# Performance work log

Measured on AMD Instinct MI355X. Metric: run time of the kernel, lower is better.

Reference implementation:

```python
import jax, jax.numpy as jnp
import numpy as np

N = 50000
E = 800000
F_IN, F_HID, F_OUT = 128, 128, 64


def setup_inputs() -> dict:
    key = jax.random.key(0)
    ks = jax.random.split(key, 8)
    x = jax.random.normal(ks[0], (N, F_IN), dtype=jnp.float32)
    attn_edge_index = jax.random.randint(ks[1], (2, E), 0, N, dtype=jnp.int64)
    attn_edge_weight = jax.random.uniform(ks[2], (E,), dtype=jnp.float32)
    # GCNConv params (glorot-ish scale); PyG lin has no bias, conv bias added after aggregation
    W1 = jax.random.normal(ks[3], (F_IN, F_HID), dtype=jnp.float32) * (1.0 / np.sqrt(F_IN))
    b1 = jnp.zeros((F_HID,), dtype=jnp.float32)
    W2 = jax.random.normal(ks[4], (F_HID, F_OUT), dtype=jnp.float32) * (1.0 / np.sqrt(F_HID))
    b2 = jnp.zeros((F_OUT,), dtype=jnp.float32)
    return {"x": x, "attn_edge_index": attn_edge_index, "attn_edge_weight": attn_edge_weight,
            "W1": W1, "b1": b1, "W2": W2, "b2": b2}


def _gcn_norm(edge_index, edge_weight, num_nodes):
    # Add self-loops with weight 1 (PyG gcn_norm default)
    loop = jnp.arange(num_nodes, dtype=edge_index.dtype)
    src = jnp.concatenate([edge_index[0], loop])
    dst = jnp.concatenate([edge_index[1], loop])
    w = jnp.concatenate([edge_weight, jnp.ones((num_nodes,), edge_weight.dtype)])
    deg = jax.ops.segment_sum(w, dst, num_segments=num_nodes)  # in-degree weighted
    dinv = jnp.where(deg > 0, jax.lax.rsqrt(deg), 0.0)
    norm = dinv[src] * w * dinv[dst]  # symmetric normalization
    return src, dst, norm


def _gcn_conv(h, src, dst, norm, W, b, num_nodes):
    h = h @ W                                   # [N, Fout] dense transform
    msg = norm[:, None] * h[src]                # [E+N, Fout] gather-multiply
    out = jax.ops.segment_sum(msg, dst, num_segments=num_nodes)  # scatter-add
    return out + b


def reference(x, attn_edge_index, attn_edge_weight, W1, b1, W2, b2):
    num_nodes = x.shape[0]
    src, dst, norm = _gcn_norm(attn_edge_index, attn_edge_weight, num_nodes)
    h = _gcn_conv(x, src, dst, norm, W1, b1, num_nodes)
    h = jax.nn.relu(h)
    # dropout(p=0.5) is identity in eval mode
    h = _gcn_conv(h, src, dst, norm, W2, b2, num_nodes)
    return h
```

## Files before the change

### kernel.cpp

```cpp
#include <hip/hip_runtime.h>
#include <hip/hip_bf16.h>

static constexpr int FIN   = 128;
static constexpr int FHID  = 128;
static constexpr int FOUTC = 64;
static constexpr int CAP   = 64;

typedef short bf16x8 __attribute__((ext_vector_type(8)));
typedef float f32x4 __attribute__((ext_vector_type(4)));

__device__ __forceinline__ float bfbits2f(unsigned short u) {
  union { unsigned i; float f; } c; c.i = ((unsigned)u) << 16; return c.f;
}
__device__ __forceinline__ float wbits2f(unsigned u) {
  union { unsigned i; float f; } c; c.i = u; return c.f;
}
__device__ __forceinline__ unsigned f2wbits(float f) {
  union { float fv; unsigned i; } c; c.fv = f; return c.i;
}
__device__ __forceinline__ void unpack_bf2(unsigned u, float& lo, float& hi) {
  union { unsigned i; float f; } a, b;
  a.i = u << 16;
  b.i = u & 0xffff0000u;
  lo = a.f; hi = b.f;
}
__device__ __forceinline__ unsigned short f2bfbits(float f) {
  union { float fv; unsigned i; } c; c.fv = f;
  unsigned i = c.i;
  unsigned r = i + 0x7FFFu + ((i >> 16) & 1u);
  if ((i & 0x7F800000u) == 0x7F800000u) r = i;
  return (unsigned short)(r >> 16);
}
__device__ __forceinline__ int ld_idx(const void* ei, int is64, long long off) {
  return is64 ? (int)((const long long*)ei)[off] : ((const int*)ei)[off];
}
__device__ __forceinline__ float ld_f(const void* p, int isbf, long long i) {
  return isbf ? bfbits2f(((const unsigned short*)p)[i]) : ((const float*)p)[i];
}

__device__ __forceinline__ int compact_row(uint2 rec, int lane, const float* __restrict__ dinv,
                                           int& rsrc, float& rw) {
  unsigned long long m = __ballot(rec.y != 0u);
  int c = __popcll(m);
  int rank = __popcll(m & ((1ull << lane) - 1ull));
  int destl = (rec.y != 0u) ? rank : c + (lane - rank);
  rsrc = __builtin_amdgcn_ds_permute(destl << 2, (int)rec.x);
  int rwb = __builtin_amdgcn_ds_permute(destl << 2, (int)rec.y);
  rw = (lane < c) ? wbits2f((unsigned)rwb) * dinv[rsrc] : 0.f;
  return c;
}

__global__ void setup_kernel(const unsigned short* __restrict__ xb,
                             const unsigned* __restrict__ eiw,
                             const void* __restrict__ W1, const void* __restrict__ W2,
                             int* __restrict__ flags, unsigned short* __restrict__ Wt1,
                             unsigned short* __restrict__ Wt2) {
  const int tid = threadIdx.x;
  __shared__ int sflags[2];
  if (tid < 64) {
    unsigned short xs = xb[2 * tid];
    unsigned long long mb = __ballot(((xs >> 7) & 0xFFu) >= 0xC0u);
    unsigned long long m2 = __ballot(eiw[2 * tid + 1] != 0u);
    if (tid == 0) {
      sflags[0] = (mb == 0ull);
      sflags[1] = (m2 == 0ull);
      if (blockIdx.x == 0) { flags[0] = sflags[0]; flags[1] = sflags[1]; }
    }
  }
  __syncthreads();
  int f = sflags[0];
  int i = blockIdx.x * 256 + tid;
  if (i < 128 * 128) {
    int k = i >> 7, nn = i & 127;
    Wt1[nn * 128 + k] = f2bfbits(ld_f(W1, f, i));
  } else {
    int j = i - 128 * 128;
    int k = j >> 6, nn = j & 63;
    Wt2[nn * 128 + k] = f2bfbits(ld_f(W2, f, j));
  }
}

__global__ void fill_ell(const void* __restrict__ ei, const void* __restrict__ ew,
                         const int* __restrict__ flg, unsigned long long* __restrict__ ell,
                         int E, int half) {
  int g = blockIdx.x * 256 + threadIdx.x;
  if (g >= half) return;
  int is64 = flg[1], isbf = flg[0];
  int sA = ld_idx(ei, is64, g);
  int dA = ld_idx(ei, is64, (long long)E + g);
  unsigned wA = f2wbits(ld_f(ew, isbf, g));
  int eB = g + half;
  bool hasB = eB < E;
  int sB = 0, dB = 0;
  unsigned wB = 0u;
  if (hasB) {
    sB = ld_idx(ei, is64, eB);
    dB = ld_idx(ei, is64, (long long)E + eB);
    wB = f2wbits(ld_f(ew, isbf, eB));
  }
  unsigned long long vA = ((unsigned long long)wA << 32) | (unsigned)sA;
  unsigned long long vB = ((unsigned long long)wB << 32) | (unsigned)sB;
  unsigned long long* rowA = ell + (size_t)dA * CAP;
  unsigned long long* rowB = ell + (size_t)dB * CAP;
  int pA = g & (CAP - 1), pB = eB & (CAP - 1);
  bool doneA = (vA == 0ull);
  bool doneB = !hasB || (vB == 0ull);
  unsigned long long oA = doneA ? 0ull : atomicCAS(&rowA[pA], 0ull, vA);
  unsigned long long oB = doneB ? 0ull : atomicCAS(&rowB[pB], 0ull, vB);
  for (int t = 1; t < CAP && !doneA && oA != 0ull; ++t) {
    pA = (pA + 1) & (CAP - 1);
    oA = atomicCAS(&rowA[pA], 0ull, vA);
  }
  for (int t = 1; t < CAP && !doneB && oB != 0ull; ++t) {
    pB = (pB + 1) & (CAP - 1);
    oB = atomicCAS(&rowB[pB], 0ull, vB);
  }
}

__global__ void node_dinv(const uint2* __restrict__ ell, float* __restrict__ dinv, int n) {
  int wid = (blockIdx.x * 256 + threadIdx.x) >> 6;
  int lane = threadIdx.x & 63;
  if (wid >= n) return;
  float w = wbits2f(ell[(size_t)wid * CAP + lane].y);
#pragma unroll
  for (int off = 1; off < 64; off <<= 1) w += __shfl_xor(w, off);
  if (lane == 0) dinv[wid] = rsqrtf(1.f + w);
}

__launch_bounds__(256)
__global__ void gather_l1(const void* __restrict__ x, const int* __restrict__ flg,
                          const uint2* __restrict__ ell, const float* __restrict__ dinv,
                          uint4* __restrict__ agg, int n) {
  int wid = (blockIdx.x * 256 + threadIdx.x) >> 6;
  int lane = threadIdx.x & 63;
  if (wid >= n) return;
  uint2 rec = ell[(size_t)wid * CAP + lane];
  int rsrc;
  float rw;
  int c = compact_row(rec, lane, dinv, rsrc, rw);
  float di = dinv[wid];

  if (flg[0]) {
    const uint4* xv = (const uint4*)x;
    const int fgrp = lane & 15, egrp = lane >> 4;
    float acc[8];
#pragma unroll
    for (int k = 0; k < 8; ++k) acc[k] = 0.f;
    int iters = (c + 15) >> 4;
    for (int it = 0; it < iters; ++it) {
      int b = it * 16 + egrp;
      int i0 = b, i1 = b + 4, i2 = b + 8, i3 = b + 12;
      int s0 = __shfl(rsrc, i0), s1 = __shfl(rsrc, i1);
      int s2 = __shfl(rsrc, i2), s3 = __shfl(rsrc, i3);
      float w0 = __shfl(rw, i0), w1 = __shfl(rw, i1);
      float w2 = __shfl(rw, i2), w3 = __shfl(rw, i3);
      s0 = i0 < c ? s0 : wid; s1 = i1 < c ? s1 : wid;
      s2 = i2 < c ? s2 : wid; s3 = i3 < c ? s3 : wid;
      uint4 u0 = xv[(size_t)s0 * 16 + fgrp];
      uint4 u1 = xv[(size_t)s1 * 16 + fgrp];
      uint4 u2 = xv[(size_t)s2 * 16 + fgrp];
      uint4 u3 = xv[(size_t)s3 * 16 + fgrp];
      float l, h;
      unpack_bf2(u0.x, l, h); acc[0] = fmaf(w0, l, acc[0]); acc[1] = fmaf(w0, h, acc[1]);
      unpack_bf2(u0.y, l, h); acc[2] = fmaf(w0, l, acc[2]); acc[3] = fmaf(w0, h, acc[3]);
      unpack_bf2(u0.z, l, h); acc[4] = fmaf(w0, l, acc[4]); acc[5] = fmaf(w0, h, acc[5]);
      unpack_bf2(u0.w, l, h); acc[6] = fmaf(w0, l, acc[6]); acc[7] = fmaf(w0, h, acc[7]);
      unpack_bf2(u1.x, l, h); acc[0] = fmaf(w1, l, acc[0]); acc[1] = fmaf(w1, h, acc[1]);
      unpack_bf2(u1.y, l, h); acc[2] = fmaf(w1, l, acc[2]); acc[3] = fmaf(w1, h, acc[3]);
      unpack_bf2(u1.z, l, h); acc[4] = fmaf(w1, l, acc[4]); acc[5] = fmaf(w1, h, acc[5]);
      unpack_bf2(u1.w, l, h); acc[6] = fmaf(w1, l, acc[6]); acc[7] = fmaf(w1, h, acc[7]);
      unpack_bf2(u2.x, l, h); acc[0] = fmaf(w2, l, acc[0]); acc[1] = fmaf(w2, h, acc[1]);
      unpack_bf2(u2.y, l, h); acc[2] = fmaf(w2, l, acc[2]); acc[3] = fmaf(w2, h, acc[3]);
      unpack_bf2(u2.z, l, h); acc[4] = fmaf(w2, l, acc[4]); acc[5] = fmaf(w2, h, acc[5]);
      unpack_bf2(u2.w, l, h); acc[6] = fmaf(w2, l, acc[6]); acc[7] = fmaf(w2, h, acc[7]);
      unpack_bf2(u3.x, l, h); acc[0] = fmaf(w3, l, acc[0]); acc[1] = fmaf(w3, h, acc[1]);
      unpack_bf2(u3.y, l, h); acc[2] = fmaf(w3, l, acc[2]); acc[3] = fmaf(w3, h, acc[3]);
      unpack_bf2(u3.z, l, h); acc[4] = fmaf(w3, l, acc[4]); acc[5] = fmaf(w3, h, acc[5]);
      unpack_bf2(u3.w, l, h); acc[6] = fmaf(w3, l, acc[6]); acc[7] = fmaf(w3, h, acc[7]);
    }
#pragma unroll
    for (int k = 0; k < 8; ++k) {
      acc[k] += __shfl_xor(acc[k], 16);
      acc[k] += __shfl_xor(acc[k], 32);
    }
    if (lane < 16) {
      uint4 su = xv[(size_t)wid * 16 + fgrp];
      float s0, s1, s2, s3, s4, s5, s6, s7;
      unpack_bf2(su.x, s0, s1); unpack_bf2(su.y, s2, s3);
      unpack_bf2(su.z, s4, s5); unpack_bf2(su.w, s6, s7);
      float dd = di * di;
      float o0 = di * acc[0] + dd * s0, o1 = di * acc[1] + dd * s1;
      float o2 = di * acc[2] + dd * s2, o3 = di * acc[3] + dd * s3;
      float o4 = di * acc[4] + dd * s4, o5 = di * acc[5] + dd * s5;
      float o6 = di * acc[6] + dd * s6, o7 = di * acc[7] + dd * s7;
      uint4 pk;
      pk.x = (unsigned)f2bfbits(o0) | ((unsigned)f2bfbits(o1) << 16);
      pk.y = (unsigned)f2bfbits(o2) | ((unsigned)f2bfbits(o3) << 16);
      pk.z = (unsigned)f2bfbits(o4) | ((unsigned)f2bfbits(o5) << 16);
      pk.w = (unsigned)f2bfbits(o6) | ((unsigned)f2bfbits(o7) << 16);
      agg[(size_t)wid * 16 + fgrp] = pk;
    }
  } else {
    const float4* xf = (const float4*)x;
    const int fgrp = lane & 31, egrp = lane >> 5;
    float acc[4] = {0.f, 0.f, 0.f, 0.f};
    int it8 = (c + 7) >> 3;
    for (int it = 0; it < it8; ++it) {
      int b = it * 8 + egrp;
#pragma unroll
      for (int t = 0; t < 4; ++t) {
        int idx = b + t * 2;
        int s = __shfl(rsrc, idx);
        float w = __shfl(rw, idx);
        s = idx < c ? s : wid;
        float4 v = xf[(size_t)s * 32 + fgrp];
        acc[0] = fmaf(w, v.x, acc[0]); acc[1] = fmaf(w, v.y, acc[1]);
        acc[2] = fmaf(w, v.z, acc[2]); acc[3] = fmaf(w, v.w, acc[3]);
      }
    }
#pragma unroll
    for (int k = 0; k < 4; ++k) acc[k] += __shfl_xor(acc[k], 32);
    if (lane < 32) {
      float4 sv = xf[(size_t)wid * 32 + fgrp];
      float dd = di * di;
      float o0 = di * acc[0] + dd * sv.x, o1 = di * acc[1] + dd * sv.y;
      float o2 = di * acc[2] + dd * sv.z, o3 = di * acc[3] + dd * sv.w;
      uint2 pk;
      pk.x = (unsigned)f2bfbits(o0) | ((unsigned)f2bfbits(o1) << 16);
      pk.y = (unsigned)f2bfbits(o2) | ((unsigned)f2bfbits(o3) << 16);
      ((uint2*)agg)[(size_t)wid * 32 + fgrp] = pk;
    }
  }
}

__launch_bounds__(256)
__global__ void gather_l2(const unsigned short* __restrict__ hw2, const int* __restrict__ flg,
                          const uint2* __restrict__ ell, const float* __restrict__ dinv,
                          const void* __restrict__ b2, void* __restrict__ out, int n) {
  int wid = (blockIdx.x * 256 + threadIdx.x) >> 6;
  int lane = threadIdx.x & 63;
  if (wid >= n) return;
  uint2 rec = ell[(size_t)wid * CAP + lane];
  int rsrc;
  float rw;
  int c = compact_row(rec, lane, dinv, rsrc, rw);
  float di = dinv[wid];

  const uint4* hv = (const uint4*)hw2;
  const int fgrp = lane & 7, egrp = lane >> 3;
  float acc[8];
#pragma unroll
  for (int k = 0; k < 8; ++k) acc[k] = 0.f;
  int iters = (c + 15) >> 4;
  for (int it = 0; it < iters; ++it) {
    int i0 = it * 16 + egrp, i1 = i0 + 8;
    int s0 = __shfl(rsrc, i0), s1 = __shfl(rsrc, i1);
    float w0 = __shfl(rw, i0), w1 = __shfl(rw, i1);
    s0 = i0 < c ? s0 : wid;
    s1 = i1 < c ? s1 : wid;
    uint4 u0 = hv[(size_t)s0 * 8 + fgrp];
    uint4 u1 = hv[(size_t)s1 * 8 + fgrp];
    float l, h;
    unpack_bf2(u0.x, l, h); acc[0] = fmaf(w0, l, acc[0]); acc[1] = fmaf(w0, h, acc[1]);
    unpack_bf2(u0.y, l, h); acc[2] = fmaf(w0, l, acc[2]); acc[3] = fmaf(w0, h, acc[3]);
    unpack_bf2(u0.z, l, h); acc[4] = fmaf(w0, l, acc[4]); acc[5] = fmaf(w0, h, acc[5]);
    unpack_bf2(u0.w, l, h); acc[6] = fmaf(w0, l, acc[6]); acc[7] = fmaf(w0, h, acc[7]);
    unpack_bf2(u1.x, l, h); acc[0] = fmaf(w1, l, acc[0]); acc[1] = fmaf(w1, h, acc[1]);
    unpack_bf2(u1.y, l, h); acc[2] = fmaf(w1, l, acc[2]); acc[3] = fmaf(w1, h, acc[3]);
    unpack_bf2(u1.z, l, h); acc[4] = fmaf(w1, l, acc[4]); acc[5] = fmaf(w1, h, acc[5]);
    unpack_bf2(u1.w, l, h); acc[6] = fmaf(w1, l, acc[6]); acc[7] = fmaf(w1, h, acc[7]);
  }
#pragma unroll
  for (int k = 0; k < 8; ++k) {
    acc[k] += __shfl_xor(acc[k], 8);
    acc[k] += __shfl_xor(acc[k], 16);
    acc[k] += __shfl_xor(acc[k], 32);
  }
  if (lane < 8) {
    int isbf = flg[0];
    uint4 su = hv[(size_t)wid * 8 + fgrp];
    float s0, s1, s2, s3, s4, s5, s6, s7;
    unpack_bf2(su.x, s0, s1); unpack_bf2(su.y, s2, s3);
    unpack_bf2(su.z, s4, s5); unpack_bf2(su.w, s6, s7);
    float dd = di * di;
    float o0 = di * acc[0] + dd * s0 + ld_f(b2, isbf, fgrp * 8 + 0);
    float o1 = di * acc[1] + dd * s1 + ld_f(b2, isbf, fgrp * 8 + 1);
    float o2 = di * acc[2] + dd * s2 + ld_f(b2, isbf, fgrp * 8 + 2);
    float o3 = di * acc[3] + dd * s3 + ld_f(b2, isbf, fgrp * 8 + 3);
    float o4 = di * acc[4] + dd * s4 + ld_f(b2, isbf, fgrp * 8 + 4);
    float o5 = di * acc[5] + dd * s5 + ld_f(b2, isbf, fgrp * 8 + 5);
    float o6 = di * acc[6] + dd * s6 + ld_f(b2, isbf, fgrp * 8 + 6);
    float o7 = di * acc[7] + dd * s7 + ld_f(b2, isbf, fgrp * 8 + 7);
    if (isbf) {
      uint4 pk;
      pk.x = (unsigned)f2bfbits(o0) | ((unsigned)f2bfbits(o1) << 16);
      pk.y = (unsigned)f2bfbits(o2) | ((unsigned)f2bfbits(o3) << 16);
      pk.z = (unsigned)f2bfbits(o4) | ((unsigned)f2bfbits(o5) << 16);
      pk.w = (unsigned)f2bfbits(o6) | ((unsigned)f2bfbits(o7) << 16);
      ((uint4*)out)[(size_t)wid * 8 + fgrp] = pk;
    } else {
      ((float4*)out)[(size_t)wid * 16 + fgrp * 2 + 0] = make_float4(o0, o1, o2, o3);
      ((float4*)out)[(size_t)wid * 16 + fgrp * 2 + 1] = make_float4(o4, o5, o6, o7);
    }
  }
}

__launch_bounds__(256)
__global__ void gemm12(const unsigned short* __restrict__ agg1,
                       const unsigned short* __restrict__ Wt1,
                       const unsigned short* __restrict__ Wt2,
                       const void* __restrict__ b1, const int* __restrict__ flg,
                       unsigned short* __restrict__ hw2, int M) {
  __shared__ unsigned short As[128 * 128];
  __shared__ unsigned short W1s[128 * 128];
  __shared__ unsigned short W2s[64 * 128];
  const int tid = threadIdx.x;
  const int r0 = blockIdx.x * 128;

  for (int i = tid; i < 128 * 16; i += 256) {
    int r = i >> 4, ch = i & 15;
    uint4 v = make_uint4(0u, 0u, 0u, 0u);
    if (r0 + r < M) v = *(const uint4*)(agg1 + (size_t)(r0 + r) * 128 + ch * 8);
    *(uint4*)&As[r * 128 + ((ch ^ (r & 15)) << 3)] = v;
  }
  for (int i = tid; i < 128 * 16; i += 256) {
    int r = i >> 4, ch = i & 15;
    uint4 v = *(const uint4*)(Wt1 + (size_t)r * 128 + ch * 8);
    *(uint4*)&W1s[r * 128 + ((ch ^ (r & 15)) << 3)] = v;
  }
  for (int i = tid; i < 64 * 16; i += 256) {
    int r = i >> 4, ch = i & 15;
    uint4 v = *(const uint4*)(Wt2 + (size_t)r * 128 + ch * 8);
    *(uint4*)&W2s[r * 128 + ((ch ^ (r & 15)) << 3)] = v;
  }
  __syncthreads();

  const int lane = tid & 63;
  const int wv = tid >> 6;
  const int ln15 = lane & 15;
  const int kq = lane >> 4;
  const int wbf = flg[0];

  f32x4 acc1[2][8];
#pragma unroll
  for (int mi = 0; mi < 2; ++mi)
#pragma unroll
    for (int nt = 0; nt < 8; ++nt) acc1[mi][nt] = (f32x4){0.f, 0.f, 0.f, 0.f};
#pragma unroll
  for (int kc = 0; kc < 4; ++kc) {
    int coff = (((kc * 4 + kq) ^ ln15) << 3);
    bf16x8 a0 = *(const bf16x8*)&As[((2 * wv + 0) * 16 + ln15) * 128 + coff];
    bf16x8 a1 = *(const bf16x8*)&As[((2 * wv + 1) * 16 + ln15) * 128 + coff];
#pragma unroll
    for (int nt = 0; nt < 8; ++nt) {
      bf16x8 b = *(const bf16x8*)&W1s[(nt * 16 + ln15) * 128 + coff];
      acc1[0][nt] = __builtin_amdgcn_mfma_f32_16x16x32_bf16(a0, b, acc1[0][nt], 0, 0, 0);
      acc1[1][nt] = __builtin_amdgcn_mfma_f32_16x16x32_bf16(a1, b, acc1[1][nt], 0, 0, 0);
    }
  }

#pragma unroll
  for (int nt = 0; nt < 8; ++nt) {
    int col = nt * 16 + ln15;
    float bv = ld_f(b1, wbf, col);
#pragma unroll
    for (int mi = 0; mi < 2; ++mi) {
#pragma unroll
      for (int r = 0; r < 4; ++r) {
        int row = 32 * wv + mi * 16 + kq * 4 + r;
        float o = fmaxf(acc1[mi][nt][r] + bv, 0.f);
        As[row * 128 + ((((col >> 3)) ^ (row & 15)) << 3) + (col & 7)] = f2bfbits(o);
      }
    }
  }
  __syncthreads();

  f32x4 acc2[2][4];
#pragma unroll
  for (int mi = 0; mi < 2; ++mi)
#pragma unroll
    for (int nt = 0; nt < 4; ++nt) acc2[mi][nt] = (f32x4){0.f, 0.f, 0.f, 0.f};
#pragma unroll
  for (int kc = 0; kc < 4; ++kc) {
    int coff = (((kc * 4 + kq) ^ ln15) << 3);
    bf16x8 a0 = *(const bf16x8*)&As[((2 * wv + 0) * 16 + ln15) * 128 + coff];
    bf16x8 a1 = *(const bf16x8*)&As[((2 * wv + 1) * 16 + ln15) * 128 + coff];
#pragma unroll
    for (int nt = 0; nt < 4; ++nt) {
      bf16x8 b = *(const bf16x8*)&W2s[(nt * 16 + ln15) * 128 + coff];
      acc2[0][nt] = __builtin_amdgcn_mfma_f32_16x16x32_bf16(a0, b, acc2[0][nt], 0, 0, 0);
      acc2[1][nt] = __builtin_amdgcn_mfma_f32_16x16x32_bf16(a1, b, acc2[1][nt], 0, 0, 0);
    }
  }
#pragma unroll
  for (int nt = 0; nt < 4; ++nt) {
    int col = nt * 16 + ln15;
#pragma unroll
    for (int mi = 0; mi < 2; ++mi) {
#pragma unroll
      for (int r = 0; r < 4; ++r) {
        int gr = r0 + 32 * wv + mi * 16 + kq * 4 + r;
        if (gr < M) hw2[(size_t)gr * 64 + col] = f2bfbits(acc2[mi][nt][r]);
      }
    }
  }
}

extern "C" void kernel_launch(void* const* d_in, const int* in_sizes, int n_in, void* d_out,
                              int out_size, void* d_ws, size_t ws_size, hipStream_t stream) {
  const void* x  = d_in[0];
  const void* ei = d_in[1];
  const void* ew = d_in[2];
  const void* W1 = d_in[3];
  const void* b1 = d_in[4];
  const void* W2 = d_in[5];
  const void* b2 = d_in[6];

  const int N = in_sizes[0] / FIN;
  const int E = in_sizes[1] / 2;
  const int B = 256;

  int* flags   = (int*)d_ws;
  float* dinv  = (float*)(flags + 16);
  unsigned short* Wt1 = (unsigned short*)(dinv + N);
  unsigned short* Wt2 = Wt1 + 128 * 128;
  unsigned long long* ell = (unsigned long long*)(Wt2 + 64 * 128);
  unsigned short* agg1 = (unsigned short*)(ell + (size_t)N * CAP);
  unsigned short* hw2  = agg1 + (size_t)N * FHID;

  const int half = (E + 1) / 2;
  hipMemsetAsync(ell, 0, (size_t)N * CAP * sizeof(unsigned long long), stream);
  setup_kernel<<<96, B, 0, stream>>>((const unsigned short*)x, (const unsigned*)ei, W1, W2,
                                     flags, Wt1, Wt2);
  fill_ell<<<(half + B - 1) / B, B, 0, stream>>>(ei, ew, flags, ell, E, half);
  node_dinv<<<(N + 3) / 4, B, 0, stream>>>((const uint2*)ell, dinv, N);
  gather_l1<<<(N + 3) / 4, B, 0, stream>>>(x, flags, (const uint2*)ell, dinv, (uint4*)agg1, N);
  gemm12<<<(N + 127) / 128, B, 0, stream>>>(agg1, Wt1, Wt2, b1, flags, hw2, N);
  gather_l2<<<(N + 3) / 4, B, 0, stream>>>(hw2, flags, (const uint2*)ell, dinv, b2, d_out, N);
}
```

Baseline: 234.8 us.

## Persistent phased layer-1 gather partitioned by source range with grid soft barriers

Replaces the one-wave-per-node layer-1 gather with a persistent kernel of 1024 blocks. Each block keeps about 49 node accumulators and compacted edge lists in LDS and walks the edges in four phases by source-node range, separated by spin-wait grid barriers, so each phase's gathered feature rows stay L2-resident. The ELL zeroing moves from hipMemsetAsync into setup_kernel, and setup_kernel also clears the barrier counters. This adds barrier spin cost, a bounded spin that can fall through without full synchronisation, edge weights rounded to bf16, and a dependence on all 1024 blocks being co-resident.

```diff
diff --git a/kernel.cpp b/kernel.cpp
--- a/kernel.cpp
+++ b/kernel.cpp
@@ -5,6 +5,9 @@
 static constexpr int FHID  = 128;
 static constexpr int FOUTC = 64;
 static constexpr int CAP   = 64;
+static constexpr int NBLK  = 1024;
+static constexpr int PN    = 49;
+static constexpr int NPH   = 4;
 
 typedef short bf16x8 __attribute__((ext_vector_type(8)));
 typedef float f32x4 __attribute__((ext_vector_type(4)));
@@ -50,12 +53,28 @@
   return c;
 }
 
+__device__ __forceinline__ void soft_barrier(int* __restrict__ ctr, int idx, int target) {
+  __syncthreads();
+  if (threadIdx.x == 0) {
+    __threadfence();
+    atomicAdd(&ctr[idx], 1);
+    for (int spins = 0; spins < 3000; ++spins) {
+      int v = __hip_atomic_load(&ctr[idx], __ATOMIC_RELAXED, __HIP_MEMORY_SCOPE_AGENT);
+      if (v >= target) break;
+      __builtin_amdgcn_s_sleep(1);
+    }
+  }
+  __syncthreads();
+}
+
 __global__ void setup_kernel(const unsigned short* __restrict__ xb,
                              const unsigned* __restrict__ eiw,
                              const void* __restrict__ W1, const void* __restrict__ W2,
                              int* __restrict__ flags, unsigned short* __restrict__ Wt1,
-                             unsigned short* __restrict__ Wt2) {
+                             unsigned short* __restrict__ Wt2, uint4* __restrict__ ellz,
+                             int nell4) {
   const int tid = threadIdx.x;
+  const int gid = blockIdx.x * 256 + tid;
   __shared__ int sflags[2];
   if (tid < 64) {
     unsigned short xs = xb[2 * tid];
@@ -67,17 +86,22 @@
       if (blockIdx.x == 0) { flags[0] = sflags[0]; flags[1] = sflags[1]; }
     }
   }
+  if (blockIdx.x == 0 && tid >= 128 && tid < 144) flags[8 + (tid - 128)] = 0;
   __syncthreads();
   int f = sflags[0];
-  int i = blockIdx.x * 256 + tid;
-  if (i < 128 * 128) {
-    int k = i >> 7, nn = i & 127;
-    Wt1[nn * 128 + k] = f2bfbits(ld_f(W1, f, i));
-  } else {
-    int j = i - 128 * 128;
-    int k = j >> 6, nn = j & 63;
-    Wt2[nn * 128 + k] = f2bfbits(ld_f(W2, f, j));
-  }
+  if (blockIdx.x < 96) {
+    int i = gid;
+    if (i < 128 * 128) {
+      int k = i >> 7, nn = i & 127;
+      Wt1[nn * 128 + k] = f2bfbits(ld_f(W1, f, i));
+    } else {
+      int j = i - 128 * 128;
+      int k = j >> 6, nn = j & 63;
+      Wt2[nn * 128 + k] = f2bfbits(ld_f(W2, f, j));
+    }
+  }
+  uint4 z = make_uint4(0u, 0u, 0u, 0u);
+  for (int j = gid; j < nell4; j += gridDim.x * 256) ellz[j] = z;
 }
 
 __global__ void fill_ell(const void* __restrict__ ei, const void* __restrict__ ew,
@@ -127,108 +151,182 @@
   if (lane == 0) dinv[wid] = rsqrtf(1.f + w);
 }
 
-__launch_bounds__(256)
-__global__ void gather_l1(const void* __restrict__ x, const int* __restrict__ flg,
-                          const uint2* __restrict__ ell, const float* __restrict__ dinv,
-                          uint4* __restrict__ agg, int n) {
-  int wid = (blockIdx.x * 256 + threadIdx.x) >> 6;
-  int lane = threadIdx.x & 63;
-  if (wid >= n) return;
-  uint2 rec = ell[(size_t)wid * CAP + lane];
-  int rsrc;
-  float rw;
-  int c = compact_row(rec, lane, dinv, rsrc, rw);
-  float di = dinv[wid];
-
-  if (flg[0]) {
-    const uint4* xv = (const uint4*)x;
-    const int fgrp = lane & 15, egrp = lane >> 4;
-    float acc[8];
-#pragma unroll
-    for (int k = 0; k < 8; ++k) acc[k] = 0.f;
-    int iters = (c + 15) >> 4;
-    for (int it = 0; it < iters; ++it) {
-      int b = it * 16 + egrp;
-      int i0 = b, i1 = b + 4, i2 = b + 8, i3 = b + 12;
-      int s0 = __shfl(rsrc, i0), s1 = __shfl(rsrc, i1);
-      int s2 = __shfl(rsrc, i2), s3 = __shfl(rsrc, i3);
-      float w0 = __shfl(rw, i0), w1 = __shfl(rw, i1);
-      float w2 = __shfl(rw, i2), w3 = __shfl(rw, i3);
-      s0 = i0 < c ? s0 : wid; s1 = i1 < c ? s1 : wid;
-      s2 = i2 < c ? s2 : wid; s3 = i3 < c ? s3 : wid;
-      uint4 u0 = xv[(size_t)s0 * 16 + fgrp];
-      uint4 u1 = xv[(size_t)s1 * 16 + fgrp];
-      uint4 u2 = xv[(size_t)s2 * 16 + fgrp];
-      uint4 u3 = xv[(size_t)s3 * 16 + fgrp];
-      float l, h;
-      unpack_bf2(u0.x, l, h); acc[0] = fmaf(w0, l, acc[0]); acc[1] = fmaf(w0, h, acc[1]);
-      unpack_bf2(u0.y, l, h); acc[2] = fmaf(w0, l, acc[2]); acc[3] = fmaf(w0, h, acc[3]);
-      unpack_bf2(u0.z, l, h); acc[4] = fmaf(w0, l, acc[4]); acc[5] = fmaf(w0, h, acc[5]);
-      unpack_bf2(u0.w, l, h); acc[6] = fmaf(w0, l, acc[6]); acc[7] = fmaf(w0, h, acc[7]);
-      unpack_bf2(u1.x, l, h); acc[0] = fmaf(w1, l, acc[0]); acc[1] = fmaf(w1, h, acc[1]);
-      unpack_bf2(u1.y, l, h); acc[2] = fmaf(w1, l, acc[2]); acc[3] = fmaf(w1, h, acc[3]);
-      unpack_bf2(u1.z, l, h); acc[4] = fmaf(w1, l, acc[4]); acc[5] = fmaf(w1, h, acc[5]);
-      unpack_bf2(u1.w, l, h); acc[6] = fmaf(w1, l, acc[6]); acc[7] = fmaf(w1, h, acc[7]);
-      unpack_bf2(u2.x, l, h); acc[0] = fmaf(w2, l, acc[0]); acc[1] = fmaf(w2, h, acc[1]);
-      unpack_bf2(u2.y, l, h); acc[2] = fmaf(w2, l, acc[2]); acc[3] = fmaf(w2, h, acc[3]);
-      unpack_bf2(u2.z, l, h); acc[4] = fmaf(w2, l, acc[4]); acc[5] = fmaf(w2, h, acc[5]);
-      unpack_bf2(u2.w, l, h); acc[6] = fmaf(w2, l, acc[6]); acc[7] = fmaf(w2, h, acc[7]);
-      unpack_bf2(u3.x, l, h); acc[0] = fmaf(w3, l, acc[0]); acc[1] = fmaf(w3, h, acc[1]);
-      unpack_bf2(u3.y, l, h); acc[2] = fmaf(w3, l, acc[2]); acc[3] = fmaf(w3, h, acc[3]);
-      unpack_bf2(u3.z, l, h); acc[4] = fmaf(w3, l, acc[4]); acc[5] = fmaf(w3, h, acc[5]);
-      unpack_bf2(u3.w, l, h); acc[6] = fmaf(w3, l, acc[6]); acc[7] = fmaf(w3, h, acc[7]);
-    }
-#pragma unroll
-    for (int k = 0; k < 8; ++k) {
-      acc[k] += __shfl_xor(acc[k], 16);
-      acc[k] += __shfl_xor(acc[k], 32);
-    }
-    if (lane < 16) {
-      uint4 su = xv[(size_t)wid * 16 + fgrp];
-      float s0, s1, s2, s3, s4, s5, s6, s7;
-      unpack_bf2(su.x, s0, s1); unpack_bf2(su.y, s2, s3);
-      unpack_bf2(su.z, s4, s5); unpack_bf2(su.w, s6, s7);
-      float dd = di * di;
-      float o0 = di * acc[0] + dd * s0, o1 = di * acc[1] + dd * s1;
-      float o2 = di * acc[2] + dd * s2, o3 = di * acc[3] + dd * s3;
-      float o4 = di * acc[4] + dd * s4, o5 = di * acc[5] + dd * s5;
-      float o6 = di * acc[6] + dd * s6, o7 = di * acc[7] + dd * s7;
-      uint4 pk;
-      pk.x = (unsigned)f2bfbits(o0) | ((unsigned)f2bfbits(o1) << 16);
-      pk.y = (unsigned)f2bfbits(o2) | ((unsigned)f2bfbits(o3) << 16);
-      pk.z = (unsigned)f2bfbits(o4) | ((unsigned)f2bfbits(o5) << 16);
-      pk.w = (unsigned)f2bfbits(o6) | ((unsigned)f2bfbits(o7) << 16);
-      agg[(size_t)wid * 16 + fgrp] = pk;
-    }
-  } else {
-    const float4* xf = (const float4*)x;
-    const int fgrp = lane & 31, egrp = lane >> 5;
-    float acc[4] = {0.f, 0.f, 0.f, 0.f};
-    int it8 = (c + 7) >> 3;
-    for (int it = 0; it < it8; ++it) {
-      int b = it * 8 + egrp;
-#pragma unroll
-      for (int t = 0; t < 4; ++t) {
-        int idx = b + t * 2;
-        int s = __shfl(rsrc, idx);
-        float w = __shfl(rw, idx);
-        s = idx < c ? s : wid;
-        float4 v = xf[(size_t)s * 32 + fgrp];
-        acc[0] = fmaf(w, v.x, acc[0]); acc[1] = fmaf(w, v.y, acc[1]);
-        acc[2] = fmaf(w, v.z, acc[2]); acc[3] = fmaf(w, v.w, acc[3]);
-      }
-    }
-#pragma unroll
-    for (int k = 0; k < 4; ++k) acc[k] += __shfl_xor(acc[k], 32);
-    if (lane < 32) {
-      float4 sv = xf[(size_t)wid * 32 + fgrp];
-      float dd = di * di;
-      float o0 = di * acc[0] + dd * sv.x, o1 = di * acc[1] + dd * sv.y;
-      float o2 = di * acc[2] + dd * sv.z, o3 = di * acc[3] + dd * sv.w;
-      uint2 pk;
-      pk.x = (unsigned)f2bfbits(o0) | ((unsigned)f2bfbits(o1) << 16);
-      pk.y = (unsigned)f2bfbits(o2) | ((unsigned)f2bfbits(o3) << 16);
-      ((uint2*)agg)[(size_t)wid * 32 + fgrp] = pk;
+__launch_bounds__(256, 4)
+__global__ void gather_l1p(const void* __restrict__ x, const int* __restrict__ flg,
+                           const uint2* __restrict__ ell, const float* __restrict__ dinv,
+                           unsigned* __restrict__ agg, int n, int* __restrict__ ctr) {
+  __shared__ float accL[PN * 128];
+  __shared__ unsigned eL[PN * CAP];
+  __shared__ int cL[PN];
+  const int tid = threadIdx.x;
+  const int wv = tid >> 6;
+  const int lane = tid & 63;
+  const int blk = blockIdx.x;
+  const int isbf = flg[0];
+
+  for (int i = wv; blk + i * NBLK < n; i += 4) {
+    int nd = blk + i * NBLK;
+    uint2 rec = ell[(size_t)nd * CAP + lane];
+    bool valid = rec.y != 0u;
+    unsigned long long m = __ballot(valid);
+    int c = __popcll(m);
+    int rank = __popcll(m & ((1ull << lane) - 1ull));
+    int destl = valid ? rank : c + (lane - rank);
+    float wdi = valid ? wbits2f(rec.y) * dinv[rec.x] : 0.f;
+    unsigned entry = ((unsigned)rec.x << 16) | (unsigned)f2bfbits(wdi);
+    int pe = __builtin_amdgcn_ds_permute(destl << 2, (int)entry);
+    if (lane < c) eL[i * CAP + lane] = (unsigned)pe;
+    if (lane == 0) cL[i] = c;
+    float di = dinv[nd];
+    if (isbf) {
+      if (lane < 16) {
+        uint4 su = ((const uint4*)x)[(size_t)nd * 16 + lane];
+        float f0, f1, f2, f3, f4, f5, f6, f7;
+        unpack_bf2(su.x, f0, f1); unpack_bf2(su.y, f2, f3);
+        unpack_bf2(su.z, f4, f5); unpack_bf2(su.w, f6, f7);
+        float* a = &accL[i * 128];
+        a[0 * 16 + lane] = di * f0; a[1 * 16 + lane] = di * f1;
+        a[2 * 16 + lane] = di * f2; a[3 * 16 + lane] = di * f3;
+        a[4 * 16 + lane] = di * f4; a[5 * 16 + lane] = di * f5;
+        a[6 * 16 + lane] = di * f6; a[7 * 16 + lane] = di * f7;
+      }
+    } else {
+      if (lane < 32) {
+        float4 sv = ((const float4*)x)[(size_t)nd * 32 + lane];
+        float* a = &accL[i * 128];
+        a[0 * 32 + lane] = di * sv.x; a[1 * 32 + lane] = di * sv.y;
+        a[2 * 32 + lane] = di * sv.z; a[3 * 32 + lane] = di * sv.w;
+      }
+    }
+  }
+
+  const int CH = (n + NPH - 1) / NPH;
+  for (int p = 0; p < NPH; ++p) {
+    soft_barrier(ctr + 8, p, NBLK);
+    int lo, hi;
+    if (isbf) { lo = p * CH; hi = lo + CH; }
+    else      { lo = (p == 0) ? 0 : n + 1; hi = (p == 0) ? n : n + 1; }
+    for (int i = wv; blk + i * NBLK < n; i += 4) {
+      int nd = blk + i * NBLK;
+      int c = cL[i];
+      unsigned e = (lane < c) ? eL[i * CAP + lane] : 0u;
+      int src = (int)(e >> 16);
+      bool act = (lane < c) && src >= lo && src < hi;
+      unsigned long long m = __ballot(act);
+      int cp = __popcll(m);
+      if (cp == 0) continue;
+      int rank = __popcll(m & ((1ull << lane) - 1ull));
+      int destl = act ? rank : cp + (lane - rank);
+      int rsrc = __builtin_amdgcn_ds_permute(destl << 2, src);
+      int rwb = __builtin_amdgcn_ds_permute(destl << 2, (int)(e << 16));
+      float rw = wbits2f((unsigned)rwb);
+
+      if (isbf) {
+        const uint4* xv = (const uint4*)x;
+        const int fgrp = lane & 15, egrp = lane >> 4;
+        float acc[8];
+#pragma unroll
+        for (int k = 0; k < 8; ++k) acc[k] = 0.f;
+        int iters = (cp + 15) >> 4;
+        for (int it = 0; it < iters; ++it) {
+          int b = it * 16 + egrp;
+          int i0 = b, i1 = b + 4, i2 = b + 8, i3 = b + 12;
+          int s0 = __shfl(rsrc, i0), s1 = __shfl(rsrc, i1);
+          int s2 = __shfl(rsrc, i2), s3 = __shfl(rsrc, i3);
+          float w0 = __shfl(rw, i0), w1 = __shfl(rw, i1);
+          float w2 = __shfl(rw, i2), w3 = __shfl(rw, i3);
+          s0 = i0 < cp ? s0 : nd; w0 = i0 < cp ? w0 : 0.f;
+          s1 = i1 < cp ? s1 : nd; w1 = i1 < cp ? w1 : 0.f;
+          s2 = i2 < cp ? s2 : nd; w2 = i2 < cp ? w2 : 0.f;
+          s3 = i3 < cp ? s3 : nd; w3 = i3 < cp ? w3 : 0.f;
+          uint4 u0 = xv[(size_t)s0 * 16 + fgrp];
+          uint4 u1 = xv[(size_t)s1 * 16 + fgrp];
+          uint4 u2 = xv[(size_t)s2 * 16 + fgrp];
+          uint4 u3 = xv[(size_t)s3 * 16 + fgrp];
+          float l, h;
+          unpack_bf2(u0.x, l, h); acc[0] = fmaf(w0, l, acc[0]); acc[1] = fmaf(w0, h, acc[1]);
+          unpack_bf2(u0.y, l, h); acc[2] = fmaf(w0, l, acc[2]); acc[3] = fmaf(w0, h, acc[3]);
+          unpack_bf2(u0.z, l, h); acc[4] = fmaf(w0, l, acc[4]); acc[5] = fmaf(w0, h, acc[5]);
+          unpack_bf2(u0.w, l, h); acc[6] = fmaf(w0, l, acc[6]); acc[7] = fmaf(w0, h, acc[7]);
+          unpack_bf2(u1.x, l, h); acc[0] = fmaf(w1, l, acc[0]); acc[1] = fmaf(w1, h, acc[1]);
+          unpack_bf2(u1.y, l, h); acc[2] = fmaf(w1, l, acc[2]); acc[3] = fmaf(w1, h, acc[3]);
+          unpack_bf2(u1.z, l, h); acc[4] = fmaf(w1, l, acc[4]); acc[5] = fmaf(w1, h, acc[5]);
+          unpack_bf2(u1.w, l, h); acc[6] = fmaf(w1, l, acc[6]); acc[7] = fmaf(w1, h, acc[7]);
+          unpack_bf2(u2.x, l, h); acc[0] = fmaf(w2, l, acc[0]); acc[1] = fmaf(w2, h, acc[1]);
+          unpack_bf2(u2.y, l, h); acc[2] = fmaf(w2, l, acc[2]); acc[3] = fmaf(w2, h, acc[3]);
+          unpack_bf2(u2.z, l, h); acc[4] = fmaf(w2, l, acc[4]); acc[5] = fmaf(w2, h, acc[5]);
+          unpack_bf2(u2.w, l, h); acc[6] = fmaf(w2, l, acc[6]); acc[7] = fmaf(w2, h, acc[7]);
+          unpack_bf2(u3.x, l, h); acc[0] = fmaf(w3, l, acc[0]); acc[1] = fmaf(w3, h, acc[1]);
+          unpack_bf2(u3.y, l, h); acc[2] = fmaf(w3, l, acc[2]); acc[3] = fmaf(w3, h, acc[3]);
+          unpack_bf2(u3.z, l, h); acc[4] = fmaf(w3, l, acc[4]); acc[5] = fmaf(w3, h, acc[5]);
+          unpack_bf2(u3.w, l, h); acc[6] = fmaf(w3, l, acc[6]); acc[7] = fmaf(w3, h, acc[7]);
+        }
+#pragma unroll
+        for (int k = 0; k < 8; ++k) {
+          acc[k] += __shfl_xor(acc[k], 16);
+          acc[k] += __shfl_xor(acc[k], 32);
+        }
+        if (lane < 16) {
+          float* a = &accL[i * 128];
+#pragma unroll
+          for (int k = 0; k < 8; ++k) a[k * 16 + fgrp] += acc[k];
+        }
+      } else {
+        const float4* xf = (const float4*)x;
+        const int fgrp = lane & 31, egrp = lane >> 5;
+        float acc[4] = {0.f, 0.f, 0.f, 0.f};
+        int it8 = (cp + 7) >> 3;
+        for (int it = 0; it < it8; ++it) {
+          int b = it * 8 + egrp;
+#pragma unroll
+          for (int t = 0; t < 4; ++t) {
+            int idx = b + t * 2;
+            int s = __shfl(rsrc, idx);
+            float w = __shfl(rw, idx);
+            s = idx < cp ? s : nd;
+            w = idx < cp ? w : 0.f;
+            float4 v = xf[(size_t)s * 32 + fgrp];
+            acc[0] = fmaf(w, v.x, acc[0]); acc[1] = fmaf(w, v.y, acc[1]);
+            acc[2] = fmaf(w, v.z, acc[2]); acc[3] = fmaf(w, v.w, acc[3]);
+          }
+        }
+#pragma unroll
+        for (int k = 0; k < 4; ++k) acc[k] += __shfl_xor(acc[k], 32);
+        if (lane < 32) {
+          float* a = &accL[i * 128];
+#pragma unroll
+          for (int k = 0; k < 4; ++k) a[k * 32 + fgrp] += acc[k];
+        }
+      }
+    }
+  }
+
+  for (int i = wv; blk + i * NBLK < n; i += 4) {
+    int nd = blk + i * NBLK;
+    float di = dinv[nd];
+    if (isbf) {
+      if (lane < 16) {
+        const float* a = &accL[i * 128];
+        float o[8];
+#pragma unroll
+        for (int k = 0; k < 8; ++k) o[k] = di * a[k * 16 + lane];
+        uint4 pk;
+        pk.x = (unsigned)f2bfbits(o[0]) | ((unsigned)f2bfbits(o[1]) << 16);
+        pk.y = (unsigned)f2bfbits(o[2]) | ((unsigned)f2bfbits(o[3]) << 16);
+        pk.z = (unsigned)f2bfbits(o[4]) | ((unsigned)f2bfbits(o[5]) << 16);
+        pk.w = (unsigned)f2bfbits(o[6]) | ((unsigned)f2bfbits(o[7]) << 16);
+        ((uint4*)agg)[(size_t)nd * 16 + lane] = pk;
+      }
+    } else {
+      if (lane < 32) {
+        const float* a = &accL[i * 128];
+        float o0 = di * a[0 * 32 + lane], o1 = di * a[1 * 32 + lane];
+        float o2 = di * a[2 * 32 + lane], o3 = di * a[3 * 32 + lane];
+        uint2 pk;
+        pk.x = (unsigned)f2bfbits(o0) | ((unsigned)f2bfbits(o1) << 16);
+        pk.y = (unsigned)f2bfbits(o2) | ((unsigned)f2bfbits(o3) << 16);
+        ((uint2*)agg)[(size_t)nd * 32 + lane] = pk;
+      }
     }
   }
 }
@@ -421,7 +519,7 @@
   const int B = 256;
 
   int* flags   = (int*)d_ws;
-  float* dinv  = (float*)(flags + 16);
+  float* dinv  = (float*)(flags + 24);
   unsigned short* Wt1 = (unsigned short*)(dinv + N);
   unsigned short* Wt2 = Wt1 + 128 * 128;
   unsigned long long* ell = (unsigned long long*)(Wt2 + 64 * 128);
@@ -429,12 +527,12 @@
   unsigned short* hw2  = agg1 + (size_t)N * FHID;
 
   const int half = (E + 1) / 2;
-  hipMemsetAsync(ell, 0, (size_t)N * CAP * sizeof(unsigned long long), stream);
-  setup_kernel<<<96, B, 0, stream>>>((const unsigned short*)x, (const unsigned*)ei, W1, W2,
-                                     flags, Wt1, Wt2);
+  setup_kernel<<<512, B, 0, stream>>>((const unsigned short*)x, (const unsigned*)ei, W1, W2,
+                                      flags, Wt1, Wt2, (uint4*)ell, N * CAP / 2);
   fill_ell<<<(half + B - 1) / B, B, 0, stream>>>(ei, ew, flags, ell, E, half);
   node_dinv<<<(N + 3) / 4, B, 0, stream>>>((const uint2*)ell, dinv, N);
-  gather_l1<<<(N + 3) / 4, B, 0, stream>>>(x, flags, (const uint2*)ell, dinv, (uint4*)agg1, N);
+  gather_l1p<<<NBLK, B, 0, stream>>>(x, flags, (const uint2*)ell, dinv, (unsigned*)agg1, N,
+                                     flags);
   gemm12<<<(N + 127) / 128, B, 0, stream>>>(agg1, Wt1, Wt2, b1, flags, hw2, N);
   gather_l2<<<(N + 3) / 4, B, 0, stream>>>(hw2, flags, (const uint2*)ell, dinv, b2, d_out, N);
 }
```

Measured after the change: 559.4 us. 138% more time.

## Precompact ELL rows into packed 32-bit edges and split layer-1 gather by feature half

Applied to the files above, without the earlier changes.

Node-degree computation now also compacts each ELL row into packed 32-bit entries, with the source index in the high 16 bits and a bf16 edge weight in the low 16. The entries are written in place over the ELL buffer, so both gathers read half the edge bytes and no longer redo the ballot/permute compaction. The layer-1 gather is split into two launches, each handling 64 features. This aims at a smaller working set per pass for better cache reuse. The ELL memset is folded into the setup kernel, and nontemporal loads and stores are used. The risks are packing that assumes fewer than 65536 nodes, weights rounded to bf16, and an extra kernel launch.

```diff
diff --git a/kernel.cpp b/kernel.cpp
--- a/kernel.cpp
+++ b/kernel.cpp
@@ -8,6 +8,8 @@
 
 typedef short bf16x8 __attribute__((ext_vector_type(8)));
 typedef float f32x4 __attribute__((ext_vector_type(4)));
+typedef unsigned u32x2 __attribute__((ext_vector_type(2)));
+typedef unsigned u32x4 __attribute__((ext_vector_type(4)));
 
 __device__ __forceinline__ float bfbits2f(unsigned short u) {
   union { unsigned i; float f; } c; c.i = ((unsigned)u) << 16; return c.f;
@@ -38,24 +40,14 @@
   return isbf ? bfbits2f(((const unsigned short*)p)[i]) : ((const float*)p)[i];
 }
 
-__device__ __forceinline__ int compact_row(uint2 rec, int lane, const float* __restrict__ dinv,
-                                           int& rsrc, float& rw) {
-  unsigned long long m = __ballot(rec.y != 0u);
-  int c = __popcll(m);
-  int rank = __popcll(m & ((1ull << lane) - 1ull));
-  int destl = (rec.y != 0u) ? rank : c + (lane - rank);
-  rsrc = __builtin_amdgcn_ds_permute(destl << 2, (int)rec.x);
-  int rwb = __builtin_amdgcn_ds_permute(destl << 2, (int)rec.y);
-  rw = (lane < c) ? wbits2f((unsigned)rwb) * dinv[rsrc] : 0.f;
-  return c;
-}
-
 __global__ void setup_kernel(const unsigned short* __restrict__ xb,
                              const unsigned* __restrict__ eiw,
                              const void* __restrict__ W1, const void* __restrict__ W2,
                              int* __restrict__ flags, unsigned short* __restrict__ Wt1,
-                             unsigned short* __restrict__ Wt2) {
+                             unsigned short* __restrict__ Wt2, uint4* __restrict__ ellz,
+                             int nell4) {
   const int tid = threadIdx.x;
+  const int gid = blockIdx.x * 256 + tid;
   __shared__ int sflags[2];
   if (tid < 64) {
     unsigned short xs = xb[2 * tid];
@@ -69,15 +61,19 @@
   }
   __syncthreads();
   int f = sflags[0];
-  int i = blockIdx.x * 256 + tid;
-  if (i < 128 * 128) {
-    int k = i >> 7, nn = i & 127;
-    Wt1[nn * 128 + k] = f2bfbits(ld_f(W1, f, i));
-  } else {
-    int j = i - 128 * 128;
-    int k = j >> 6, nn = j & 63;
-    Wt2[nn * 128 + k] = f2bfbits(ld_f(W2, f, j));
-  }
+  if (blockIdx.x < 96) {
+    int i = gid;
+    if (i < 128 * 128) {
+      int k = i >> 7, nn = i & 127;
+      Wt1[nn * 128 + k] = f2bfbits(ld_f(W1, f, i));
+    } else {
+      int j = i - 128 * 128;
+      int k = j >> 6, nn = j & 63;
+      Wt2[nn * 128 + k] = f2bfbits(ld_f(W2, f, j));
+    }
+  }
+  uint4 z = make_uint4(0u, 0u, 0u, 0u);
+  for (int j = gid; j < nell4; j += gridDim.x * 256) ellz[j] = z;
 }
 
 __global__ void fill_ell(const void* __restrict__ ei, const void* __restrict__ ew,
@@ -117,49 +113,59 @@
   }
 }
 
-__global__ void node_dinv(const uint2* __restrict__ ell, float* __restrict__ dinv, int n) {
+__global__ void dinv_compact(uint2* __restrict__ ell, float* __restrict__ dinv,
+                             unsigned* __restrict__ cedge, int n) {
   int wid = (blockIdx.x * 256 + threadIdx.x) >> 6;
   int lane = threadIdx.x & 63;
   if (wid >= n) return;
-  float w = wbits2f(ell[(size_t)wid * CAP + lane].y);
-#pragma unroll
-  for (int off = 1; off < 64; off <<= 1) w += __shfl_xor(w, off);
-  if (lane == 0) dinv[wid] = rsqrtf(1.f + w);
-}
-
+  u32x2 rv = __builtin_nontemporal_load((const u32x2*)(ell + (size_t)wid * CAP) + lane);
+  float w = wbits2f(rv.y);
+  float ws = w;
+#pragma unroll
+  for (int off = 1; off < 64; off <<= 1) ws += __shfl_xor(ws, off);
+  bool valid = rv.y != 0u;
+  unsigned long long m = __ballot(valid);
+  int c = __popcll(m);
+  int rank = __popcll(m & ((1ull << lane) - 1ull));
+  int destl = valid ? rank : c + (lane - rank);
+  unsigned entry = valid ? ((rv.x << 16) | (unsigned)f2bfbits(w)) : 0u;
+  int pe = __builtin_amdgcn_ds_permute(destl << 2, (int)entry);
+  cedge[(size_t)wid * (CAP * 2) + lane] = (unsigned)pe;
+  if (lane == 0) dinv[wid] = rsqrtf(1.f + ws);
+}
+
+template <int PASS>
 __launch_bounds__(256)
-__global__ void gather_l1(const void* __restrict__ x, const int* __restrict__ flg,
-                          const uint2* __restrict__ ell, const float* __restrict__ dinv,
-                          uint4* __restrict__ agg, int n) {
+__global__ void gather_l1h(const void* __restrict__ x, const int* __restrict__ flg,
+                           const unsigned* __restrict__ cedge, const float* __restrict__ dinv,
+                           unsigned* __restrict__ agg, int n) {
   int wid = (blockIdx.x * 256 + threadIdx.x) >> 6;
   int lane = threadIdx.x & 63;
   if (wid >= n) return;
-  uint2 rec = ell[(size_t)wid * CAP + lane];
-  int rsrc;
-  float rw;
-  int c = compact_row(rec, lane, dinv, rsrc, rw);
+  const int isbf = flg[0];
+  if (!isbf && PASS == 1) return;
+  unsigned e = cedge[(size_t)wid * (CAP * 2) + lane];
+  unsigned long long m = __ballot(e != 0u);
+  int c = __popcll(m);
+  int rsrc = (int)(e >> 16);
+  float rw = (lane < c) ? bfbits2f((unsigned short)(e & 0xFFFFu)) * dinv[rsrc] : 0.f;
   float di = dinv[wid];
 
-  if (flg[0]) {
+  if (isbf) {
     const uint4* xv = (const uint4*)x;
-    const int fgrp = lane & 15, egrp = lane >> 4;
+    const int fgrp = lane & 7, egrp = lane >> 3, cofs = PASS * 8;
     float acc[8];
 #pragma unroll
     for (int k = 0; k < 8; ++k) acc[k] = 0.f;
     int iters = (c + 15) >> 4;
     for (int it = 0; it < iters; ++it) {
-      int b = it * 16 + egrp;
-      int i0 = b, i1 = b + 4, i2 = b + 8, i3 = b + 12;
+      int i0 = it * 16 + egrp, i1 = i0 + 8;
       int s0 = __shfl(rsrc, i0), s1 = __shfl(rsrc, i1);
-      int s2 = __shfl(rsrc, i2), s3 = __shfl(rsrc, i3);
       float w0 = __shfl(rw, i0), w1 = __shfl(rw, i1);
-      float w2 = __shfl(rw, i2), w3 = __shfl(rw, i3);
-      s0 = i0 < c ? s0 : wid; s1 = i1 < c ? s1 : wid;
-      s2 = i2 < c ? s2 : wid; s3 = i3 < c ? s3 : wid;
-      uint4 u0 = xv[(size_t)s0 * 16 + fgrp];
-      uint4 u1 = xv[(size_t)s1 * 16 + fgrp];
-      uint4 u2 = xv[(size_t)s2 * 16 + fgrp];
-      uint4 u3 = xv[(size_t)s3 * 16 + fgrp];
+      s0 = i0 < c ? s0 : wid;
+      s1 = i1 < c ? s1 : wid;
+      uint4 u0 = xv[(size_t)s0 * 16 + cofs + fgrp];
+      uint4 u1 = xv[(size_t)s1 * 16 + cofs + fgrp];
       float l, h;
       unpack_bf2(u0.x, l, h); acc[0] = fmaf(w0, l, acc[0]); acc[1] = fmaf(w0, h, acc[1]);
       unpack_bf2(u0.y, l, h); acc[2] = fmaf(w0, l, acc[2]); acc[3] = fmaf(w0, h, acc[3]);
@@ -169,22 +175,15 @@
       unpack_bf2(u1.y, l, h); acc[2] = fmaf(w1, l, acc[2]); acc[3] = fmaf(w1, h, acc[3]);
       unpack_bf2(u1.z, l, h); acc[4] = fmaf(w1, l, acc[4]); acc[5] = fmaf(w1, h, acc[5]);
       unpack_bf2(u1.w, l, h); acc[6] = fmaf(w1, l, acc[6]); acc[7] = fmaf(w1, h, acc[7]);
-      unpack_bf2(u2.x, l, h); acc[0] = fmaf(w2, l, acc[0]); acc[1] = fmaf(w2, h, acc[1]);
-      unpack_bf2(u2.y, l, h); acc[2] = fmaf(w2, l, acc[2]); acc[3] = fmaf(w2, h, acc[3]);
-      unpack_bf2(u2.z, l, h); acc[4] = fmaf(w2, l, acc[4]); acc[5] = fmaf(w2, h, acc[5]);
-      unpack_bf2(u2.w, l, h); acc[6] = fmaf(w2, l, acc[6]); acc[7] = fmaf(w2, h, acc[7]);
-      unpack_bf2(u3.x, l, h); acc[0] = fmaf(w3, l, acc[0]); acc[1] = fmaf(w3, h, acc[1]);
-      unpack_bf2(u3.y, l, h); acc[2] = fmaf(w3, l, acc[2]); acc[3] = fmaf(w3, h, acc[3]);
-      unpack_bf2(u3.z, l, h); acc[4] = fmaf(w3, l, acc[4]); acc[5] = fmaf(w3, h, acc[5]);
-      unpack_bf2(u3.w, l, h); acc[6] = fmaf(w3, l, acc[6]); acc[7] = fmaf(w3, h, acc[7]);
     }
 #pragma unroll
     for (int k = 0; k < 8; ++k) {
+      acc[k] += __shfl_xor(acc[k], 8);
       acc[k] += __shfl_xor(acc[k], 16);
       acc[k] += __shfl_xor(acc[k], 32);
     }
-    if (lane < 16) {
-      uint4 su = xv[(size_t)wid * 16 + fgrp];
+    if (lane < 8) {
+      uint4 su = xv[(size_t)wid * 16 + cofs + fgrp];
       float s0, s1, s2, s3, s4, s5, s6, s7;
       unpack_bf2(su.x, s0, s1); unpack_bf2(su.y, s2, s3);
       unpack_bf2(su.z, s4, s5); unpack_bf2(su.w, s6, s7);
@@ -193,12 +192,12 @@
       float o2 = di * acc[2] + dd * s2, o3 = di * acc[3] + dd * s3;
       float o4 = di * acc[4] + dd * s4, o5 = di * acc[5] + dd * s5;
       float o6 = di * acc[6] + dd * s6, o7 = di * acc[7] + dd * s7;
-      uint4 pk;
+      u32x4 pk;
       pk.x = (unsigned)f2bfbits(o0) | ((unsigned)f2bfbits(o1) << 16);
       pk.y = (unsigned)f2bfbits(o2) | ((unsigned)f2bfbits(o3) << 16);
       pk.z = (unsigned)f2bfbits(o4) | ((unsigned)f2bfbits(o5) << 16);
       pk.w = (unsigned)f2bfbits(o6) | ((unsigned)f2bfbits(o7) << 16);
-      agg[(size_t)wid * 16 + fgrp] = pk;
+      __builtin_nontemporal_store(pk, (u32x4*)agg + (size_t)wid * 16 + cofs + fgrp);
     }
   } else {
     const float4* xf = (const float4*)x;
@@ -235,15 +234,16 @@
 
 __launch_bounds__(256)
 __global__ void gather_l2(const unsigned short* __restrict__ hw2, const int* __restrict__ flg,
-                          const uint2* __restrict__ ell, const float* __restrict__ dinv,
+                          const unsigned* __restrict__ cedge, const float* __restrict__ dinv,
                           const void* __restrict__ b2, void* __restrict__ out, int n) {
   int wid = (blockIdx.x * 256 + threadIdx.x) >> 6;
   int lane = threadIdx.x & 63;
   if (wid >= n) return;
-  uint2 rec = ell[(size_t)wid * CAP + lane];
-  int rsrc;
-  float rw;
-  int c = compact_row(rec, lane, dinv, rsrc, rw);
+  unsigned e = __builtin_nontemporal_load(cedge + (size_t)wid * (CAP * 2) + lane);
+  unsigned long long m = __ballot(e != 0u);
+  int c = __popcll(m);
+  int rsrc = (int)(e >> 16);
+  float rw = (lane < c) ? bfbits2f((unsigned short)(e & 0xFFFFu)) * dinv[rsrc] : 0.f;
   float di = dinv[wid];
 
   const uint4* hv = (const uint4*)hw2;
@@ -425,16 +425,17 @@
   unsigned short* Wt1 = (unsigned short*)(dinv + N);
   unsigned short* Wt2 = Wt1 + 128 * 128;
   unsigned long long* ell = (unsigned long long*)(Wt2 + 64 * 128);
+  unsigned* cedge = (unsigned*)ell;
   unsigned short* agg1 = (unsigned short*)(ell + (size_t)N * CAP);
   unsigned short* hw2  = agg1 + (size_t)N * FHID;
 
   const int half = (E + 1) / 2;
-  hipMemsetAsync(ell, 0, (size_t)N * CAP * sizeof(unsigned long long), stream);
-  setup_kernel<<<96, B, 0, stream>>>((const unsigned short*)x, (const unsigned*)ei, W1, W2,
-                                     flags, Wt1, Wt2);
+  setup_kernel<<<512, B, 0, stream>>>((const unsigned short*)x, (const unsigned*)ei, W1, W2,
+                                      flags, Wt1, Wt2, (uint4*)ell, N * CAP / 2);
   fill_ell<<<(half + B - 1) / B, B, 0, stream>>>(ei, ew, flags, ell, E, half);
-  node_dinv<<<(N + 3) / 4, B, 0, stream>>>((const uint2*)ell, dinv, N);
-  gather_l1<<<(N + 3) / 4, B, 0, stream>>>(x, flags, (const uint2*)ell, dinv, (uint4*)agg1, N);
+  dinv_compact<<<(N + 3) / 4, B, 0, stream>>>((uint2*)ell, dinv, cedge, N);
+  gather_l1h<0><<<(N + 3) / 4, B, 0, stream>>>(x, flags, cedge, dinv, (unsigned*)agg1, N);
+  gather_l1h<1><<<(N + 3) / 4, B, 0, stream>>>(x, flags, cedge, dinv, (unsigned*)agg1, N);
   gemm12<<<(N + 127) / 128, B, 0, stream>>>(agg1, Wt1, Wt2, b1, flags, hw2, N);
-  gather_l2<<<(N + 3) / 4, B, 0, stream>>>(hw2, flags, (const uint2*)ell, dinv, b2, d_out, N);
-}
+  gather_l2<<<(N + 3) / 4, B, 0, stream>>>(hw2, flags, cedge, dinv, b2, d_out, N);
+}
```

Result: no change. 233.1 us (-0.7%).
